# Performance work log

Hardware: AMD Instinct MI355X
Metric: run time of the kernel (lower is better)

The kernel has to match this reference:

```python
import jax, jax.numpy as jnp
import numpy as np

B, L, C = 4, 2048, 512          # batches (equal counts), seq len per cloud, d_model
DIN, DS, DCONV, DTR = 1024, 16, 4, 32  # expand*C, d_state, d_conv, dt_rank
N = B * L
EPS = 1e-5


def setup_inputs() -> dict:
    key = jax.random.key(0)
    ks = jax.random.split(key, 20)
    def n(k, shape, s=0.02):
        return jax.random.normal(k, shape, jnp.float32) * s
    p = jax.random.normal(ks[0], (N, 3), jnp.float32)
    x = jax.random.normal(ks[1], (N, C), jnp.float32)
    o = jnp.arange(1, B + 1, dtype=jnp.int32) * L  # cumulative offsets
    # hilbert serialization stand-in: a permutation within each batch segment
    r = jax.random.uniform(ks[2], (B, L))
    order = (jnp.argsort(r, axis=1) + jnp.arange(B)[:, None] * L).reshape(-1)
    inv = jnp.argsort(order)
    return dict(
        p=p, x=x, o=o, order=order, inv=inv,
        W_in=n(ks[3], (C, C)),
        bn_in_gamma=jnp.ones((C,), jnp.float32), bn_in_beta=jnp.zeros((C,), jnp.float32),
        bn_in_mean=n(ks[4], (C,), 0.1), bn_in_var=jnp.abs(n(ks[5], (C,), 0.1)) + 1.0,
        in_proj_w=n(ks[6], (2 * DIN, C)),
        conv_w=n(ks[7], (DIN, 1, DCONV), 0.2), conv_b=n(ks[8], (DIN,), 0.02),
        x_proj_w=n(ks[9], (DTR + 2 * DS, DIN)),
        dt_proj_w=n(ks[10], (DIN, DTR), 0.1), dt_proj_b=n(ks[11], (DIN,), 0.1),
        A_log=jnp.log(jnp.tile(jnp.arange(1, DS + 1, dtype=jnp.float32), (DIN, 1))),
        D=jnp.ones((DIN,), jnp.float32),
        out_proj_w=n(ks[12], (C, DIN)),
        W_out=n(ks[13], (C, C)),
        bn_out_gamma=jnp.ones((C,), jnp.float32), bn_out_beta=jnp.zeros((C,), jnp.float32),
        bn_out_mean=n(ks[14], (C,), 0.1), bn_out_var=jnp.abs(n(ks[15], (C,), 0.1)) + 1.0,
    )


def _bn(x, g, b, m, v):  # BatchNorm1d, eval semantics
    return (x - m) * jax.lax.rsqrt(v + EPS) * g + b


def _mamba(xp, in_proj_w, conv_w, conv_b, x_proj_w, dt_proj_w, dt_proj_b, A_log, D, out_proj_w):
    # xp: (B, L, C)
    xz = jnp.einsum('blc,ec->ble', xp, in_proj_w)            # (B,L,2*DIN)
    xm, z = jnp.split(xz, 2, axis=-1)
    # depthwise causal conv over sequence, truncated to L
    xc = jax.lax.conv_general_dilated(
        xm.swapaxes(1, 2), conv_w, (1,), [(DCONV - 1, 0)],
        feature_group_count=DIN, dimension_numbers=('NCH', 'OIH', 'NCH'))
    xc = jax.nn.silu(xc.swapaxes(1, 2) + conv_b)             # (B,L,DIN)
    dbl = jnp.einsum('bld,ed->ble', xc, x_proj_w)            # (B,L,DTR+2*DS)
    dt_low, Bm, Cm = jnp.split(dbl, [DTR, DTR + DS], axis=-1)
    dt = jax.nn.softplus(jnp.einsum('blr,dr->bld', dt_low, dt_proj_w) + dt_proj_b)
    A = -jnp.exp(A_log)                                      # (DIN,DS)

    def step(h, xs):
        dt_t, B_t, C_t, u_t = xs                             # (B,DIN),(B,DS),(B,DS),(B,DIN)
        dA = jnp.exp(dt_t[..., None] * A)                    # (B,DIN,DS)
        h = dA * h + dt_t[..., None] * B_t[:, None, :] * u_t[..., None]
        return h, jnp.einsum('bds,bs->bd', h, C_t)

    h0 = jnp.zeros((xp.shape[0], DIN, DS), xp.dtype)
    _, ys = jax.lax.scan(step, h0, (dt.swapaxes(0, 1), Bm.swapaxes(0, 1),
                                    Cm.swapaxes(0, 1), xc.swapaxes(0, 1)))
    y = ys.swapaxes(0, 1) + xc * D
    y = y * jax.nn.silu(z)
    return jnp.einsum('bld,cd->blc', y, out_proj_w)          # (B,L,C)


def reference(p, x, o, order, inv, W_in, bn_in_gamma, bn_in_beta, bn_in_mean, bn_in_var,
              in_proj_w, conv_w, conv_b, x_proj_w, dt_proj_w, dt_proj_b, A_log, D,
              out_proj_w, W_out, bn_out_gamma, bn_out_beta, bn_out_mean, bn_out_var):
    identity = x
    h = jax.nn.relu(_bn(x @ W_in.T, bn_in_gamma, bn_in_beta, bn_in_mean, bn_in_var))
    # serialize (gather), split into equal-length sequences (pad is empty)
    xp = h[order].reshape(B, L, C)
    y = _mamba(xp, in_proj_w, conv_w, conv_b, x_proj_w, dt_proj_w, dt_proj_b,
               A_log, D, out_proj_w)
    hs = y.reshape(N, C)[inv]                                # unpad + inverse gather
    out = _bn(hs @ W_out.T, bn_out_gamma, bn_out_beta, bn_out_mean, bn_out_var)
    return jax.nn.relu(out + identity)
```

## Files before the change

kernel.cpp:

```cpp
#include <hip/hip_runtime.h>
#include <math.h>

#define NPTS 8192
#define CDIM 512
#define LSEQ 2048
#define BATCH 4
#define DIN 1024
#define DS 16
#define DTR 32
#define EPS 1e-5f

#define LCHUNK 32
#define NCHUNK (LSEQ / LCHUNK)
#define KSPLIT 8

typedef __attribute__((ext_vector_type(8))) short bf16x8;
typedef __attribute__((ext_vector_type(4))) float f32x4;

__device__ __forceinline__ unsigned short f2bf(float f) {
  unsigned u = __float_as_uint(f);
  unsigned r = (u + 0x7fffu + ((u >> 16) & 1u)) >> 16;
  return (unsigned short)r;
}
__device__ __forceinline__ float bf2f(unsigned short b) {
  return __uint_as_float(((unsigned)b) << 16);
}

__device__ __forceinline__ void gload_lds16(const void* g, void* l) {
  __builtin_amdgcn_global_load_lds(
      (const __attribute__((address_space(1))) unsigned int*)g,
      (__attribute__((address_space(3))) unsigned int*)l, 16, 0, 0);
}

__global__ __launch_bounds__(256) void f2bf_all(
    const float* __restrict__ xsrc, unsigned short* __restrict__ xdst,
    const float* __restrict__ w0, const float* __restrict__ w1,
    const float* __restrict__ w2, const float* __restrict__ w3,
    const float* __restrict__ w4, const float* __restrict__ w5,
    unsigned short* __restrict__ wdst) {
  const int nx = NPTS * CDIM;
  const int n0 = 262144, n1 = 1048576, n2 = 524288, n3 = 262144, n4 = 65536;
  int i4 = blockIdx.x * 256 + threadIdx.x;
  int i = i4 * 4;
  const float* src;
  unsigned short* dst;
  if (i < nx) {
    src = xsrc + i;
    dst = xdst + i;
  } else {
    int j = i - nx;
    dst = wdst + j;
    if (j < n0) src = w0 + j;
    else {
      j -= n0;
      if (j < n1) src = w1 + j;
      else {
        j -= n1;
        if (j < n2) src = w2 + j;
        else {
          j -= n2;
          if (j < n3) src = w3 + j;
          else {
            j -= n3;
            if (j < n4) src = w4 + j;
            else { j -= n4; src = w5 + j; }
          }
        }
      }
    }
  }
  float4 v = *(const float4*)src;
  ushort4 o;
  o.x = f2bf(v.x); o.y = f2bf(v.y); o.z = f2bf(v.z); o.w = f2bf(v.w);
  *(ushort4*)dst = o;
}

template <int EPI>
__global__ __launch_bounds__(256) void gemm128(
    const unsigned short* __restrict__ A, int lda,
    const unsigned short* __restrict__ W,
    void* __restrict__ Cout, int N, int K,
    const int* __restrict__ rowidx, void* __restrict__ out2) {
  __shared__ __align__(16) unsigned short As[128 * 32];
  __shared__ __align__(16) unsigned short Bs[128 * 32];
  const int tid = threadIdx.x;
  const int lane = tid & 63;
  const int wave = tid >> 6;
  const int wr = wave >> 1, wc = wave & 1;
  const int bn0 = blockIdx.x * 128;
  const int bm0 = blockIdx.y * 128;

  const unsigned short* aptr[2];
  const unsigned short* bptr[2];
  unsigned short* lA[2];
  unsigned short* lB[2];
#pragma unroll
  for (int j = 0; j < 2; ++j) {
    const int r16 = (wave * 2 + j) * 16;
    const int srow = r16 + (lane >> 2);
    const int scol = (lane & 3) * 8;
    int ar = bm0 + srow;
    if (rowidx) ar = rowidx[ar];
    aptr[j] = A + (size_t)ar * lda + scol;
    bptr[j] = W + (size_t)(bn0 + srow) * K + scol;
    lA[j] = As + r16 * 32;
    lB[j] = Bs + r16 * 32;
  }

  const int l15 = lane & 15, lq = lane >> 4;
  int aoff[4], boff[4];
#pragma unroll
  for (int i = 0; i < 4; ++i) {
    aoff[i] = (wr * 64 + i * 16 + l15) * 32 + lq * 8;
    boff[i] = (wc * 64 + i * 16 + l15) * 32 + lq * 8;
  }

  f32x4 acc[4][4] = {};
  for (int k0 = 0; k0 < K; k0 += 32) {
#pragma unroll
    for (int j = 0; j < 2; ++j) {
      gload_lds16(aptr[j] + k0, lA[j]);
      gload_lds16(bptr[j] + k0, lB[j]);
    }
    __syncthreads();
    bf16x8 af[4], bfr[4];
#pragma unroll
    for (int i = 0; i < 4; ++i) {
      af[i] = *(const bf16x8*)(As + aoff[i]);
      bfr[i] = *(const bf16x8*)(Bs + boff[i]);
    }
#pragma unroll
    for (int mi = 0; mi < 4; ++mi)
#pragma unroll
      for (int ni = 0; ni < 4; ++ni)
        acc[mi][ni] = __builtin_amdgcn_mfma_f32_16x16x32_bf16(
            af[mi], bfr[ni], acc[mi][ni], 0, 0, 0);
    __syncthreads();
  }

#pragma unroll
  for (int mi = 0; mi < 4; ++mi)
#pragma unroll
    for (int ni = 0; ni < 4; ++ni)
#pragma unroll
      for (int r = 0; r < 4; ++r) {
        const int m = bm0 + wr * 64 + mi * 16 + lq * 4 + r;
        const int n = bn0 + wc * 64 + ni * 16 + l15;
        float v = acc[mi][ni][r];
        if (EPI == 4) {
          if (bn0 < 1024)
            ((unsigned short*)Cout)[(size_t)m * 1024 + n] = f2bf(v);
          else
            ((unsigned short*)out2)[(size_t)m * 1024 + (n - 1024)] = f2bf(v);
        }
      }
}

template <int EPI>
__global__ __launch_bounds__(256) void gemm12864(
    const unsigned short* __restrict__ A, int lda,
    const unsigned short* __restrict__ W,
    void* __restrict__ Cout, int N, int K,
    const int* __restrict__ rowidx,
    const float* __restrict__ e0, const float* __restrict__ e1,
    const float* __restrict__ e2, const float* __restrict__ e3,
    const float* __restrict__ resid) {
  __shared__ __align__(16) unsigned short As[128 * 32];
  __shared__ __align__(16) unsigned short Bs[64 * 32];
  const int tid = threadIdx.x;
  const int lane = tid & 63;
  const int wave = tid >> 6;
  const int bn0 = blockIdx.x * 64;
  const int bm0 = blockIdx.y * 128;

  const unsigned short* aptr[2];
  unsigned short* lA[2];
#pragma unroll
  for (int j = 0; j < 2; ++j) {
    const int r16 = (wave * 2 + j) * 16;
    const int srow = r16 + (lane >> 2);
    const int scol = (lane & 3) * 8;
    int ar = bm0 + srow;
    if (rowidx) ar = rowidx[ar];
    aptr[j] = A + (size_t)ar * lda + scol;
    lA[j] = As + r16 * 32;
  }
  const int br16 = wave * 16;
  const unsigned short* bptr = W + (size_t)(bn0 + br16 + (lane >> 2)) * K + (lane & 3) * 8;
  unsigned short* lB = Bs + br16 * 32;

  const int l15 = lane & 15, lq = lane >> 4;
  int aoff[2], boff[4];
#pragma unroll
  for (int i = 0; i < 2; ++i) aoff[i] = (wave * 32 + i * 16 + l15) * 32 + lq * 8;
#pragma unroll
  for (int i = 0; i < 4; ++i) boff[i] = (i * 16 + l15) * 32 + lq * 8;

  f32x4 acc[2][4] = {};
  for (int k0 = 0; k0 < K; k0 += 32) {
#pragma unroll
    for (int j = 0; j < 2; ++j) gload_lds16(aptr[j] + k0, lA[j]);
    gload_lds16(bptr + k0, lB);
    __syncthreads();
    bf16x8 af[2], bfr[4];
#pragma unroll
    for (int i = 0; i < 2; ++i) af[i] = *(const bf16x8*)(As + aoff[i]);
#pragma unroll
    for (int i = 0; i < 4; ++i) bfr[i] = *(const bf16x8*)(Bs + boff[i]);
#pragma unroll
    for (int mi = 0; mi < 2; ++mi)
#pragma unroll
      for (int ni = 0; ni < 4; ++ni)
        acc[mi][ni] = __builtin_amdgcn_mfma_f32_16x16x32_bf16(
            af[mi], bfr[ni], acc[mi][ni], 0, 0, 0);
    __syncthreads();
  }

#pragma unroll
  for (int mi = 0; mi < 2; ++mi)
#pragma unroll
    for (int ni = 0; ni < 4; ++ni)
#pragma unroll
      for (int r = 0; r < 4; ++r) {
        const int m = bm0 + wave * 32 + mi * 16 + lq * 4 + r;
        const int n = bn0 + ni * 16 + l15;
        float v = acc[mi][ni][r];
        if (EPI == 1) {
          v = (v - e2[n]) * rsqrtf(e3[n] + EPS) * e0[n] + e1[n];
          v = fmaxf(v, 0.f);
          ((unsigned short*)Cout)[(size_t)m * N + n] = f2bf(v);
        } else if (EPI == 2) {
          ((unsigned short*)Cout)[(size_t)m * N + n] = f2bf(v);
        } else if (EPI == 3) {
          v = (v - e2[n]) * rsqrtf(e3[n] + EPS) * e0[n] + e1[n];
          v += resid[(size_t)m * N + n];
          ((float*)Cout)[(size_t)m * N + n] = fmaxf(v, 0.f);
        }
      }
}

template <int EPI>
__global__ __launch_bounds__(256) void gemm_mfma(
    const unsigned short* __restrict__ A, int lda,
    const unsigned short* __restrict__ W,
    void* __restrict__ Cout, int N, int K,
    const float* __restrict__ e0) {
  __shared__ __align__(16) unsigned short As[64 * 32];
  __shared__ __align__(16) unsigned short Bs[64 * 32];
  const int tid = threadIdx.x;
  const int lane = tid & 63;
  const int wave = tid >> 6;
  const int wr = wave >> 1, wc = wave & 1;
  const int bn0 = blockIdx.x * 64;
  const int bm0 = blockIdx.y * 64;

  const int srow = tid >> 2;
  const int scol = (tid & 3) * 8;
  const unsigned short* aptr = A + (size_t)(bm0 + srow) * lda + scol;
  const unsigned short* bptr = W + (size_t)(bn0 + srow) * K + scol;
  unsigned short* lA = As + wave * 512;
  unsigned short* lB = Bs + wave * 512;

  const int l15 = lane & 15, lq = lane >> 4;
  int aoff[2], boff[2];
#pragma unroll
  for (int i = 0; i < 2; ++i) {
    aoff[i] = (wr * 32 + i * 16 + l15) * 32 + lq * 8;
    boff[i] = (wc * 32 + i * 16 + l15) * 32 + lq * 8;
  }

  f32x4 acc[2][2] = {};
  for (int k0 = 0; k0 < K; k0 += 32) {
    gload_lds16(aptr + k0, lA);
    gload_lds16(bptr + k0, lB);
    __syncthreads();
    bf16x8 af[2], bfr[2];
#pragma unroll
    for (int i = 0; i < 2; ++i) {
      af[i] = *(const bf16x8*)(As + aoff[i]);
      bfr[i] = *(const bf16x8*)(Bs + boff[i]);
    }
#pragma unroll
    for (int mi = 0; mi < 2; ++mi)
#pragma unroll
      for (int ni = 0; ni < 2; ++ni)
        acc[mi][ni] = __builtin_amdgcn_mfma_f32_16x16x32_bf16(
            af[mi], bfr[ni], acc[mi][ni], 0, 0, 0);
    __syncthreads();
  }

#pragma unroll
  for (int mi = 0; mi < 2; ++mi)
#pragma unroll
    for (int ni = 0; ni < 2; ++ni)
#pragma unroll
      for (int r = 0; r < 4; ++r) {
        const int m = bm0 + wr * 32 + mi * 16 + lq * 4 + r;
        const int n = bn0 + wc * 32 + ni * 16 + l15;
        float v = acc[mi][ni][r];
        if (EPI == 5) {
          v += e0[n];
          v = (v > 20.f) ? v : log1pf(expf(v));
          ((unsigned short*)Cout)[(size_t)m * N + n] = f2bf(v);
        }
      }
}

__global__ __launch_bounds__(256) void gemm_splitk(
    const unsigned short* __restrict__ A,
    const unsigned short* __restrict__ W,
    float* __restrict__ part) {
  __shared__ __align__(16) unsigned short As[64 * 32];
  __shared__ __align__(16) unsigned short Bs[64 * 32];
  const int tid = threadIdx.x;
  const int lane = tid & 63;
  const int wave = tid >> 6;
  const int wr = wave >> 1, wc = wave & 1;
  const int ks = blockIdx.x;
  const int bm0 = blockIdx.y * 64;
  const int kbase = ks * (DIN / KSPLIT);

  const int srow = tid >> 2;
  const int scol = (tid & 3) * 8;
  const unsigned short* aptr = A + (size_t)(bm0 + srow) * DIN + kbase + scol;
  const unsigned short* bptr = W + (size_t)srow * DIN + kbase + scol;
  unsigned short* lA = As + wave * 512;
  unsigned short* lB = Bs + wave * 512;

  const int l15 = lane & 15, lq = lane >> 4;
  int aoff[2], boff[2];
#pragma unroll
  for (int i = 0; i < 2; ++i) {
    aoff[i] = (wr * 32 + i * 16 + l15) * 32 + lq * 8;
    boff[i] = (wc * 32 + i * 16 + l15) * 32 + lq * 8;
  }

  f32x4 acc[2][2] = {};
#pragma unroll
  for (int k0 = 0; k0 < DIN / KSPLIT; k0 += 32) {
    gload_lds16(aptr + k0, lA);
    gload_lds16(bptr + k0, lB);
    __syncthreads();
    bf16x8 af[2], bfr[2];
#pragma unroll
    for (int i = 0; i < 2; ++i) {
      af[i] = *(const bf16x8*)(As + aoff[i]);
      bfr[i] = *(const bf16x8*)(Bs + boff[i]);
    }
#pragma unroll
    for (int mi = 0; mi < 2; ++mi)
#pragma unroll
      for (int ni = 0; ni < 2; ++ni)
        acc[mi][ni] = __builtin_amdgcn_mfma_f32_16x16x32_bf16(
            af[mi], bfr[ni], acc[mi][ni], 0, 0, 0);
    __syncthreads();
  }

  float* pbase = part + (size_t)ks * NPTS * 64;
#pragma unroll
  for (int mi = 0; mi < 2; ++mi)
#pragma unroll
    for (int ni = 0; ni < 2; ++ni)
#pragma unroll
      for (int r = 0; r < 4; ++r) {
        const int m = bm0 + wr * 32 + mi * 16 + lq * 4 + r;
        const int n = wc * 32 + ni * 16 + l15;
        pbase[(size_t)m * 64 + n] = acc[mi][ni][r];
      }
}

__global__ __launch_bounds__(256) void reduce_dbl(
    const float* __restrict__ part, float* __restrict__ dbl,
    unsigned short* __restrict__ dtlow_bf) {
  const int i4 = blockIdx.x * 256 + threadIdx.x;
  float4 s = make_float4(0.f, 0.f, 0.f, 0.f);
#pragma unroll
  for (int k = 0; k < KSPLIT; ++k) {
    float4 p = ((const float4*)(part + (size_t)k * NPTS * 64))[i4];
    s.x += p.x; s.y += p.y; s.z += p.z; s.w += p.w;
  }
  ((float4*)dbl)[i4] = s;
  const int col = (i4 * 4) & 63;
  if (col < 32) {
    ushort4 o;
    o.x = f2bf(s.x); o.y = f2bf(s.y); o.z = f2bf(s.z); o.w = f2bf(s.w);
    const int row = i4 >> 4;
    *(ushort4*)(dtlow_bf + (size_t)row * 32 + col) = o;
  }
}

__global__ __launch_bounds__(256) void conv_silu8(const unsigned short* __restrict__ xm,
                                                  const float* __restrict__ w,
                                                  const float* __restrict__ bias,
                                                  unsigned short* __restrict__ xc) {
  const int idx = blockIdx.x * 256 + threadIdx.x;
  const int dblk = idx & (DIN / 8 - 1);
  const int row = idx >> 7;
  const int d0 = dblk * 8;
  const int l = row & (LSEQ - 1);
  float acc[8];
  float4 wv[8];
#pragma unroll
  for (int j = 0; j < 8; ++j) {
    acc[j] = bias[d0 + j];
    wv[j] = *(const float4*)(w + (d0 + j) * 4);
  }
#pragma unroll
  for (int k = 0; k < 4; ++k) {
    const int ls = l - 3 + k;
    if (ls >= 0) {
      const ushort4* p = (const ushort4*)(xm + (size_t)(row - 3 + k) * DIN + d0);
      ushort4 v0 = p[0], v1 = p[1];
      const float wk[8] = {((const float*)&wv[0])[k], ((const float*)&wv[1])[k],
                           ((const float*)&wv[2])[k], ((const float*)&wv[3])[k],
                           ((const float*)&wv[4])[k], ((const float*)&wv[5])[k],
                           ((const float*)&wv[6])[k], ((const float*)&wv[7])[k]};
      acc[0] += bf2f(v0.x) * wk[0]; acc[1] += bf2f(v0.y) * wk[1];
      acc[2] += bf2f(v0.z) * wk[2]; acc[3] += bf2f(v0.w) * wk[3];
      acc[4] += bf2f(v1.x) * wk[4]; acc[5] += bf2f(v1.y) * wk[5];
      acc[6] += bf2f(v1.z) * wk[6]; acc[7] += bf2f(v1.w) * wk[7];
    }
  }
  ushort4 o0, o1;
  float t;
  t = acc[0]; t = t / (1.f + __expf(-t)); o0.x = f2bf(t);
  t = acc[1]; t = t / (1.f + __expf(-t)); o0.y = f2bf(t);
  t = acc[2]; t = t / (1.f + __expf(-t)); o0.z = f2bf(t);
  t = acc[3]; t = t / (1.f + __expf(-t)); o0.w = f2bf(t);
  t = acc[4]; t = t / (1.f + __expf(-t)); o1.x = f2bf(t);
  t = acc[5]; t = t / (1.f + __expf(-t)); o1.y = f2bf(t);
  t = acc[6]; t = t / (1.f + __expf(-t)); o1.z = f2bf(t);
  t = acc[7]; t = t / (1.f + __expf(-t)); o1.w = f2bf(t);
  ushort4* q = (ushort4*)(xc + (size_t)row * DIN + d0);
  q[0] = o0; q[1] = o1;
}

__global__ __launch_bounds__(256) void scan_passA(
    const unsigned short* __restrict__ dtb, const float* __restrict__ dbl,
    const unsigned short* __restrict__ xc, const float* __restrict__ A_log,
    unsigned short* __restrict__ S, float* __restrict__ sumdt) {
  __shared__ __align__(16) float Bsh[LCHUNK * 16];
  const int blk = blockIdx.x;
  const int dg = blk & 3;
  const int c = (blk >> 2) & (NCHUNK - 1);
  const int b = blk >> 8;
  const int d = dg * 256 + threadIdx.x;
  const size_t row0 = (size_t)b * LSEQ + (size_t)c * LCHUNK;

  if (threadIdx.x < 128) {
    const int r = threadIdx.x >> 2, q = threadIdx.x & 3;
    *(float4*)(Bsh + r * 16 + q * 4) = *(const float4*)(dbl + (row0 + r) * 64 + 32 + q * 4);
  }

  const float A0 = -__expf(A_log[d * DS]);
  float h[DS];
#pragma unroll
  for (int s = 0; s < DS; ++s) h[s] = 0.f;
  float sdt = 0.f;

  float dtp[2], up[2];
  dtp[0] = bf2f(dtb[row0 * DIN + d]);
  up[0] = bf2f(xc[row0 * DIN + d]);
  dtp[1] = bf2f(dtb[(row0 + 1) * DIN + d]);
  up[1] = bf2f(xc[(row0 + 1) * DIN + d]);
  __syncthreads();

  for (int t = 0; t < LCHUNK; ++t) {
    const float dtv = dtp[t & 1], u = up[t & 1];
    if (t + 2 < LCHUNK) {
      dtp[t & 1] = bf2f(dtb[(row0 + t + 2) * DIN + d]);
      up[t & 1] = bf2f(xc[(row0 + t + 2) * DIN + d]);
    }
    sdt += dtv;
    const float du = dtv * u;
    const float p = __expf(dtv * A0);
    float wdk = 1.f;
    const float4* B4 = (const float4*)(Bsh + t * 16);
#pragma unroll
    for (int q = 0; q < 4; ++q) {
      float4 Bv = B4[q];
      wdk *= p; h[q * 4 + 0] = wdk * h[q * 4 + 0] + du * Bv.x;
      wdk *= p; h[q * 4 + 1] = wdk * h[q * 4 + 1] + du * Bv.y;
      wdk *= p; h[q * 4 + 2] = wdk * h[q * 4 + 2] + du * Bv.z;
      wdk *= p; h[q * 4 + 3] = wdk * h[q * 4 + 3] + du * Bv.w;
    }
  }
  const size_t sb = ((size_t)(b * NCHUNK + c) * DIN + d) * DS;
#pragma unroll
  for (int q = 0; q < 4; ++q) {
    ushort4 o;
    o.x = f2bf(h[q * 4 + 0]); o.y = f2bf(h[q * 4 + 1]);
    o.z = f2bf(h[q * 4 + 2]); o.w = f2bf(h[q * 4 + 3]);
    *(ushort4*)(S + sb + q * 4) = o;
  }
  sumdt[(size_t)(b * NCHUNK + c) * DIN + d] = sdt;
}

__global__ __launch_bounds__(256) void scan_passB(
    unsigned short* __restrict__ S, const float* __restrict__ sumdt,
    const float* __restrict__ A_log) {
  const int tid = blockIdx.x * 256 + threadIdx.x;
  const int s = tid & (DS - 1);
  const int d = (tid >> 4) & (DIN - 1);
  const int b = tid >> 14;
  const float A = -__expf(A_log[d * DS + s]);
  const size_t step = (size_t)DIN * DS;
  size_t base = ((size_t)(b * NCHUNK) * DIN + d) * DS + s;
  size_t sbase = (size_t)(b * NCHUNK) * DIN + d;
  unsigned short sc = S[base];
  float sd = sumdt[sbase];
  float H = 0.f;
  for (int c = 0; c < NCHUNK; ++c) {
    unsigned short scn = 0;
    float sdn = 0.f;
    if (c + 1 < NCHUNK) {
      scn = S[base + step];
      sdn = sumdt[sbase + DIN];
    }
    const float scv = bf2f(sc);
    S[base] = f2bf(H);
    H = __expf(A * sd) * H + scv;
    base += step; sbase += DIN; sc = scn; sd = sdn;
  }
}

__global__ __launch_bounds__(256) void scan_passC(
    const unsigned short* __restrict__ dtb, const float* __restrict__ dbl,
    const unsigned short* __restrict__ xc, const unsigned short* __restrict__ zbf,
    const float* __restrict__ A_log, const float* __restrict__ Dvec,
    const unsigned short* __restrict__ S, unsigned short* __restrict__ ybf) {
  __shared__ __align__(16) float BCsh[LCHUNK * 32];
  const int blk = blockIdx.x;
  const int dg = blk & 3;
  const int c = (blk >> 2) & (NCHUNK - 1);
  const int b = blk >> 8;
  const int d = dg * 256 + threadIdx.x;
  const size_t row0 = (size_t)b * LSEQ + (size_t)c * LCHUNK;

  {
    const int r = threadIdx.x >> 3, q = threadIdx.x & 7;
    *(float4*)(BCsh + r * 32 + q * 4) = *(const float4*)(dbl + (row0 + r) * 64 + 32 + q * 4);
  }

  const float A0 = -__expf(A_log[d * DS]);
  float h[DS];
  const size_t sb = ((size_t)(b * NCHUNK + c) * DIN + d) * DS;
#pragma unroll
  for (int q = 0; q < 4; ++q) {
    ushort4 v = *(const ushort4*)(S + sb + q * 4);
    h[q * 4 + 0] = bf2f(v.x); h[q * 4 + 1] = bf2f(v.y);
    h[q * 4 + 2] = bf2f(v.z); h[q * 4 + 3] = bf2f(v.w);
  }
  const float Dv = Dvec[d];

  float dtp[2], up[2], zp[2];
  dtp[0] = bf2f(dtb[row0 * DIN + d]);
  up[0] = bf2f(xc[row0 * DIN + d]);
  zp[0] = bf2f(zbf[row0 * DIN + d]);
  dtp[1] = bf2f(dtb[(row0 + 1) * DIN + d]);
  up[1] = bf2f(xc[(row0 + 1) * DIN + d]);
  zp[1] = bf2f(zbf[(row0 + 1) * DIN + d]);
  __syncthreads();

  for (int t = 0; t < LCHUNK; ++t) {
    const size_t row = row0 + t;
    const float dtv = dtp[t & 1], u = up[t & 1], zv = zp[t & 1];
    if (t + 2 < LCHUNK) {
      dtp[t & 1] = bf2f(dtb[(row + 2) * DIN + d]);
      up[t & 1] = bf2f(xc[(row + 2) * DIN + d]);
      zp[t & 1] = bf2f(zbf[(row + 2) * DIN + d]);
    }
    const float du = dtv * u;
    const float p = __expf(dtv * A0);
    float wdk = 1.f;
    const float4* B4 = (const float4*)(BCsh + t * 32);
    const float4* C4 = (const float4*)(BCsh + t * 32 + 16);
    float y = 0.f;
#pragma unroll
    for (int q = 0; q < 4; ++q) {
      float4 Bv = B4[q];
      float4 Cv = C4[q];
      wdk *= p; h[q * 4 + 0] = wdk * h[q * 4 + 0] + du * Bv.x;
      wdk *= p; h[q * 4 + 1] = wdk * h[q * 4 + 1] + du * Bv.y;
      wdk *= p; h[q * 4 + 2] = wdk * h[q * 4 + 2] + du * Bv.z;
      wdk *= p; h[q * 4 + 3] = wdk * h[q * 4 + 3] + du * Bv.w;
      y += h[q * 4 + 0] * Cv.x + h[q * 4 + 1] * Cv.y +
           h[q * 4 + 2] * Cv.z + h[q * 4 + 3] * Cv.w;
    }
    ybf[row * DIN + d] = f2bf((y + u * Dv) * (zv / (1.f + __expf(-zv))));
  }
}

extern "C" void kernel_launch(void* const* d_in, const int* in_sizes, int n_in,
                              void* d_out, int out_size, void* d_ws, size_t ws_size,
                              hipStream_t stream) {
  const float* x = (const float*)d_in[1];
  const int* order = (const int*)d_in[3];
  const int* inv = (const int*)d_in[4];
  const float* W_in = (const float*)d_in[5];
  const float* g_in = (const float*)d_in[6];
  const float* b_in = (const float*)d_in[7];
  const float* m_in = (const float*)d_in[8];
  const float* v_in = (const float*)d_in[9];
  const float* in_proj_w = (const float*)d_in[10];
  const float* conv_w = (const float*)d_in[11];
  const float* conv_b = (const float*)d_in[12];
  const float* x_proj_w = (const float*)d_in[13];
  const float* dt_proj_w = (const float*)d_in[14];
  const float* dt_proj_b = (const float*)d_in[15];
  const float* A_log = (const float*)d_in[16];
  const float* Dvec = (const float*)d_in[17];
  const float* out_proj_w = (const float*)d_in[18];
  const float* W_out = (const float*)d_in[19];
  const float* g_out = (const float*)d_in[20];
  const float* b_out = (const float*)d_in[21];
  const float* m_out = (const float*)d_in[22];
  const float* v_out = (const float*)d_in[23];
  float* out = (float*)d_out;

  char* cur = (char*)d_ws;
  unsigned short* xm_bf = (unsigned short*)cur; cur += (size_t)NPTS * DIN * 2;
  unsigned short* zbf = (unsigned short*)cur; cur += (size_t)NPTS * DIN * 2;
  unsigned short* xc_bf = (unsigned short*)cur; cur += (size_t)NPTS * DIN * 2;
  float* dbl = (float*)cur; cur += (size_t)NPTS * 64 * 4;
  unsigned short* dtlow_bf = (unsigned short*)cur; cur += (size_t)NPTS * 32 * 2;
  unsigned short* dt_bf = (unsigned short*)cur; cur += (size_t)NPTS * DIN * 2;
  float* part = (float*)cur; cur += (size_t)KSPLIT * NPTS * 64 * 4;
  unsigned short* r1 = (unsigned short*)cur; cur += (size_t)NPTS * DIN * 2;
  unsigned short* r2 = (unsigned short*)cur; cur += (size_t)NPTS * CDIM * 2;
  unsigned short* W_in_bf = (unsigned short*)cur; cur += 512 * 512 * 2;
  unsigned short* in_proj_bf = (unsigned short*)cur; cur += 2048 * 512 * 2;
  unsigned short* out_proj_bf = (unsigned short*)cur; cur += 512 * 1024 * 2;
  unsigned short* W_out_bf = (unsigned short*)cur; cur += 512 * 512 * 2;
  unsigned short* x_proj_bf = (unsigned short*)cur; cur += 64 * 1024 * 2;
  unsigned short* dt_proj_bf = (unsigned short*)cur; cur += 1024 * 32 * 2;
  unsigned short* x_bf = r1;
  unsigned short* y_bf = r1;
  unsigned short* h_bf = r2;
  unsigned short* out1_bf = r2;
  unsigned short* S = (unsigned short*)part;
  float* sumdt = (float*)xm_bf;

  dim3 blk(256);
  f2bf_all<<<dim3((NPTS * CDIM + 2195456) / 4 / 256), blk, 0, stream>>>(
      x, x_bf, W_in, in_proj_w, out_proj_w, W_out, x_proj_w, dt_proj_w, W_in_bf);

  gemm12864<1><<<dim3(CDIM / 64, NPTS / 128), blk, 0, stream>>>(
      x_bf, CDIM, W_in_bf, h_bf, CDIM, CDIM, nullptr, g_in, b_in, m_in, v_in, nullptr);
  gemm128<4><<<dim3(2048 / 128, NPTS / 128), blk, 0, stream>>>(
      h_bf, CDIM, in_proj_bf, xm_bf, 2048, CDIM, order, zbf);
  conv_silu8<<<dim3(NPTS * DIN / 8 / 256), blk, 0, stream>>>(xm_bf, conv_w, conv_b, xc_bf);
  gemm_splitk<<<dim3(KSPLIT, NPTS / 64), blk, 0, stream>>>(xc_bf, x_proj_bf, part);
  reduce_dbl<<<dim3(NPTS * 64 / 4 / 256), blk, 0, stream>>>(part, dbl, dtlow_bf);
  gemm_mfma<5><<<dim3(DIN / 64, NPTS / 64), blk, 0, stream>>>(
      dtlow_bf, 32, dt_proj_bf, dt_bf, DIN, 32, dt_proj_b);
  scan_passA<<<dim3(BATCH * NCHUNK * (DIN / 256)), blk, 0, stream>>>(
      dt_bf, dbl, xc_bf, A_log, S, sumdt);
  scan_passB<<<dim3(BATCH * DIN * DS / 256), blk, 0, stream>>>(S, sumdt, A_log);
  scan_passC<<<dim3(BATCH * NCHUNK * (DIN / 256)), blk, 0, stream>>>(
      dt_bf, dbl, xc_bf, zbf, A_log, Dvec, S, y_bf);
  gemm12864<2><<<dim3(CDIM / 64, NPTS / 128), blk, 0, stream>>>(
      y_bf, DIN, out_proj_bf, out1_bf, CDIM, DIN, nullptr, nullptr, nullptr,
      nullptr, nullptr, nullptr);
  gemm12864<3><<<dim3(CDIM / 64, NPTS / 128), blk, 0, stream>>>(
      out1_bf, CDIM, W_out_bf, out, CDIM, CDIM, inv, g_out, b_out, m_out, v_out, x);
}
```

Before: 347.4 us.

## Fold out_proj and W_out into one weight, fuse x conversion into GEMM

Precomputes a combined weight Wc = diag(bn scale)·W_out·out_proj in a small GEMM, so the two final GEMMs collapse into one GEMM over y with the inverse gather, BN shift and residual in the epilogue. The first GEMM now reads fp32 x directly and converts it to bf16 while staging into LDS, which removes the separate activation conversion pass. It also halves KSPLIT for the x_proj split-K GEMM. In exchange, the fp32 A path uses plain register loads instead of direct global-to-LDS loads, and the folded weight is rounded to bf16, which slightly changes the numerics.

```diff
diff --git a/kernel.cpp b/kernel.cpp
--- a/kernel.cpp
+++ b/kernel.cpp
@@ -12,9 +12,10 @@
 
 #define LCHUNK 32
 #define NCHUNK (LSEQ / LCHUNK)
-#define KSPLIT 8
+#define KSPLIT 4
 
 typedef __attribute__((ext_vector_type(8))) short bf16x8;
+typedef __attribute__((ext_vector_type(8))) unsigned short u16x8;
 typedef __attribute__((ext_vector_type(4))) float f32x4;
 
 __device__ __forceinline__ unsigned short f2bf(float f) {
@@ -32,47 +33,52 @@
       (__attribute__((address_space(3))) unsigned int*)l, 16, 0, 0);
 }
 
-__global__ __launch_bounds__(256) void f2bf_all(
-    const float* __restrict__ xsrc, unsigned short* __restrict__ xdst,
+__global__ __launch_bounds__(256) void f2bf_weights(
     const float* __restrict__ w0, const float* __restrict__ w1,
     const float* __restrict__ w2, const float* __restrict__ w3,
     const float* __restrict__ w4, const float* __restrict__ w5,
-    unsigned short* __restrict__ wdst) {
-  const int nx = NPTS * CDIM;
+    unsigned short* __restrict__ dst) {
   const int n0 = 262144, n1 = 1048576, n2 = 524288, n3 = 262144, n4 = 65536;
   int i4 = blockIdx.x * 256 + threadIdx.x;
   int i = i4 * 4;
-  const float* src;
-  unsigned short* dst;
-  if (i < nx) {
-    src = xsrc + i;
-    dst = xdst + i;
-  } else {
-    int j = i - nx;
-    dst = wdst + j;
-    if (j < n0) src = w0 + j;
-    else {
-      j -= n0;
-      if (j < n1) src = w1 + j;
-      else {
-        j -= n1;
-        if (j < n2) src = w2 + j;
-        else {
-          j -= n2;
-          if (j < n3) src = w3 + j;
-          else {
-            j -= n3;
-            if (j < n4) src = w4 + j;
-            else { j -= n4; src = w5 + j; }
-          }
-        }
-      }
-    }
-  }
-  float4 v = *(const float4*)src;
-  ushort4 o;
-  o.x = f2bf(v.x); o.y = f2bf(v.y); o.z = f2bf(v.z); o.w = f2bf(v.w);
-  *(ushort4*)dst = o;
+  int j = i;
+  if (j < n0) {
+    float4 v = *(const float4*)(w0 + j);
+    *(ushort4*)(dst + i) = make_ushort4(f2bf(v.x), f2bf(v.y), f2bf(v.z), f2bf(v.w));
+    return;
+  }
+  j -= n0;
+  if (j < n1) {
+    float4 v = *(const float4*)(w1 + j);
+    *(ushort4*)(dst + i) = make_ushort4(f2bf(v.x), f2bf(v.y), f2bf(v.z), f2bf(v.w));
+    return;
+  }
+  j -= n1;
+  if (j < n2) {
+    float4 v = *(const float4*)(w2 + j);
+    const int c = j >> 10, d = j & 1023;
+    unsigned short* base = dst + n0 + n1;
+    base[(size_t)(d + 0) * 512 + c] = f2bf(v.x);
+    base[(size_t)(d + 1) * 512 + c] = f2bf(v.y);
+    base[(size_t)(d + 2) * 512 + c] = f2bf(v.z);
+    base[(size_t)(d + 3) * 512 + c] = f2bf(v.w);
+    return;
+  }
+  j -= n2;
+  if (j < n3) {
+    float4 v = *(const float4*)(w3 + j);
+    *(ushort4*)(dst + i) = make_ushort4(f2bf(v.x), f2bf(v.y), f2bf(v.z), f2bf(v.w));
+    return;
+  }
+  j -= n3;
+  if (j < n4) {
+    float4 v = *(const float4*)(w4 + j);
+    *(ushort4*)(dst + i) = make_ushort4(f2bf(v.x), f2bf(v.y), f2bf(v.z), f2bf(v.w));
+    return;
+  }
+  j -= n4;
+  float4 v = *(const float4*)(w5 + j);
+  *(ushort4*)(dst + i) = make_ushort4(f2bf(v.x), f2bf(v.y), f2bf(v.z), f2bf(v.w));
 }
 
 template <int EPI>
@@ -156,9 +162,9 @@
       }
 }
 
-template <int EPI>
+template <int EPI, int AF32>
 __global__ __launch_bounds__(256) void gemm12864(
-    const unsigned short* __restrict__ A, int lda,
+    const void* __restrict__ Av, int lda,
     const unsigned short* __restrict__ W,
     void* __restrict__ Cout, int N, int K,
     const int* __restrict__ rowidx,
@@ -167,6 +173,8 @@
     const float* __restrict__ resid) {
   __shared__ __align__(16) unsigned short As[128 * 32];
   __shared__ __align__(16) unsigned short Bs[64 * 32];
+  const unsigned short* Ab = (const unsigned short*)Av;
+  const float* Af = (const float*)Av;
   const int tid = threadIdx.x;
   const int lane = tid & 63;
   const int wave = tid >> 6;
@@ -174,6 +182,7 @@
   const int bm0 = blockIdx.y * 128;
 
   const unsigned short* aptr[2];
+  const float* aptrf[2];
   unsigned short* lA[2];
 #pragma unroll
   for (int j = 0; j < 2; ++j) {
@@ -182,7 +191,8 @@
     const int scol = (lane & 3) * 8;
     int ar = bm0 + srow;
     if (rowidx) ar = rowidx[ar];
-    aptr[j] = A + (size_t)ar * lda + scol;
+    if (AF32) aptrf[j] = Af + (size_t)ar * lda + scol;
+    else aptr[j] = Ab + (size_t)ar * lda + scol;
     lA[j] = As + r16 * 32;
   }
   const int br16 = wave * 16;
@@ -198,8 +208,20 @@
 
   f32x4 acc[2][4] = {};
   for (int k0 = 0; k0 < K; k0 += 32) {
-#pragma unroll
-    for (int j = 0; j < 2; ++j) gload_lds16(aptr[j] + k0, lA[j]);
+    if (AF32) {
+#pragma unroll
+      for (int j = 0; j < 2; ++j) {
+        const float* ap = aptrf[j] + k0;
+        float4 v0 = *(const float4*)ap;
+        float4 v1 = *(const float4*)(ap + 4);
+        u16x8 o = {f2bf(v0.x), f2bf(v0.y), f2bf(v0.z), f2bf(v0.w),
+                   f2bf(v1.x), f2bf(v1.y), f2bf(v1.z), f2bf(v1.w)};
+        *(u16x8*)(lA[j] + (size_t)lane * 8) = o;
+      }
+    } else {
+#pragma unroll
+      for (int j = 0; j < 2; ++j) gload_lds16(aptr[j] + k0, lA[j]);
+    }
     gload_lds16(bptr + k0, lB);
     __syncthreads();
     bf16x8 af[2], bfr[4];
@@ -231,8 +253,12 @@
           ((unsigned short*)Cout)[(size_t)m * N + n] = f2bf(v);
         } else if (EPI == 2) {
           ((unsigned short*)Cout)[(size_t)m * N + n] = f2bf(v);
-        } else if (EPI == 3) {
-          v = (v - e2[n]) * rsqrtf(e3[n] + EPS) * e0[n] + e1[n];
+        } else if (EPI == 6) {
+          v *= e0[m] * rsqrtf(e3[m] + EPS);
+          ((unsigned short*)Cout)[(size_t)m * N + n] = f2bf(v);
+        } else if (EPI == 7) {
+          const float s = e0[n] * rsqrtf(e3[n] + EPS);
+          v += e1[n] - e2[n] * s;
           v += resid[(size_t)m * N + n];
           ((float*)Cout)[(size_t)m * N + n] = fmaxf(v, 0.f);
         }
@@ -626,27 +652,27 @@
   unsigned short* dtlow_bf = (unsigned short*)cur; cur += (size_t)NPTS * 32 * 2;
   unsigned short* dt_bf = (unsigned short*)cur; cur += (size_t)NPTS * DIN * 2;
   float* part = (float*)cur; cur += (size_t)KSPLIT * NPTS * 64 * 4;
-  unsigned short* r1 = (unsigned short*)cur; cur += (size_t)NPTS * DIN * 2;
-  unsigned short* r2 = (unsigned short*)cur; cur += (size_t)NPTS * CDIM * 2;
+  unsigned short* y_bf = (unsigned short*)cur; cur += (size_t)NPTS * DIN * 2;
+  unsigned short* h_bf = (unsigned short*)cur; cur += (size_t)NPTS * CDIM * 2;
   unsigned short* W_in_bf = (unsigned short*)cur; cur += 512 * 512 * 2;
   unsigned short* in_proj_bf = (unsigned short*)cur; cur += 2048 * 512 * 2;
-  unsigned short* out_proj_bf = (unsigned short*)cur; cur += 512 * 1024 * 2;
+  unsigned short* out_projT_bf = (unsigned short*)cur; cur += 1024 * 512 * 2;
   unsigned short* W_out_bf = (unsigned short*)cur; cur += 512 * 512 * 2;
   unsigned short* x_proj_bf = (unsigned short*)cur; cur += 64 * 1024 * 2;
   unsigned short* dt_proj_bf = (unsigned short*)cur; cur += 1024 * 32 * 2;
-  unsigned short* x_bf = r1;
-  unsigned short* y_bf = r1;
-  unsigned short* h_bf = r2;
-  unsigned short* out1_bf = r2;
+  unsigned short* Wc_bf = (unsigned short*)cur; cur += 512 * 1024 * 2;
   unsigned short* S = (unsigned short*)part;
   float* sumdt = (float*)xm_bf;
 
   dim3 blk(256);
-  f2bf_all<<<dim3((NPTS * CDIM + 2195456) / 4 / 256), blk, 0, stream>>>(
-      x, x_bf, W_in, in_proj_w, out_proj_w, W_out, x_proj_w, dt_proj_w, W_in_bf);
-
-  gemm12864<1><<<dim3(CDIM / 64, NPTS / 128), blk, 0, stream>>>(
-      x_bf, CDIM, W_in_bf, h_bf, CDIM, CDIM, nullptr, g_in, b_in, m_in, v_in, nullptr);
+  f2bf_weights<<<dim3(2195456 / 4 / 256), blk, 0, stream>>>(
+      W_in, in_proj_w, out_proj_w, W_out, x_proj_w, dt_proj_w, W_in_bf);
+  gemm12864<6, 0><<<dim3(1024 / 64, 512 / 128), blk, 0, stream>>>(
+      W_out_bf, 512, out_projT_bf, Wc_bf, 1024, 512, nullptr,
+      g_out, nullptr, nullptr, v_out, nullptr);
+
+  gemm12864<1, 1><<<dim3(CDIM / 64, NPTS / 128), blk, 0, stream>>>(
+      x, CDIM, W_in_bf, h_bf, CDIM, CDIM, nullptr, g_in, b_in, m_in, v_in, nullptr);
   gemm128<4><<<dim3(2048 / 128, NPTS / 128), blk, 0, stream>>>(
       h_bf, CDIM, in_proj_bf, xm_bf, 2048, CDIM, order, zbf);
   conv_silu8<<<dim3(NPTS * DIN / 8 / 256), blk, 0, stream>>>(xm_bf, conv_w, conv_b, xc_bf);
@@ -659,9 +685,6 @@
   scan_passB<<<dim3(BATCH * DIN * DS / 256), blk, 0, stream>>>(S, sumdt, A_log);
   scan_passC<<<dim3(BATCH * NCHUNK * (DIN / 256)), blk, 0, stream>>>(
       dt_bf, dbl, xc_bf, zbf, A_log, Dvec, S, y_bf);
-  gemm12864<2><<<dim3(CDIM / 64, NPTS / 128), blk, 0, stream>>>(
-      y_bf, DIN, out_proj_bf, out1_bf, CDIM, DIN, nullptr, nullptr, nullptr,
-      nullptr, nullptr, nullptr);
-  gemm12864<3><<<dim3(CDIM / 64, NPTS / 128), blk, 0, stream>>>(
-      out1_bf, CDIM, W_out_bf, out, CDIM, CDIM, inv, g_out, b_out, m_out, v_out, x);
-}
+  gemm12864<7, 0><<<dim3(CDIM / 64, NPTS / 128), blk, 0, stream>>>(
+      y_bf, DIN, Wc_bf, out, CDIM, DIN, inv, g_out, b_out, m_out, v_out, x);
+}
```

New measurement: 349.8 us. Within noise of the previous version (+0.7%).
